# Kernel optimization log

Hardware: AMD Instinct MI355X
Metric: run time of the kernel (lower is better)

The kernel has to match this reference:

```python
import jax, jax.numpy as jnp
import numpy as np
from math import pi as PI

L = 8192      # sequence length
D = 512       # feature dim
EMAS = 8      # number of decay rates


def setup_inputs() -> dict:
    key = jax.random.key(0)
    k1, _ = jax.random.split(key)
    x = jax.random.normal(k1, (L, D), dtype=jnp.float32)
    # module initializes log_decay = linspace(-pi, pi, emas)
    log_decay = jnp.linspace(-PI, PI, EMAS, dtype=jnp.float32)
    return {"x": x, "log_decay": log_decay}


def reference(x, log_decay):
    decay = jax.nn.sigmoid(log_decay)               # (emas,)
    # initial state: first element broadcast over emas -> (D, emas)
    state = jnp.broadcast_to(x[0][..., None], x.shape[1:] + (EMAS,))

    def ema_step(ema_0, x_1):
        ema_1 = decay * x_1 + (1.0 - decay) * ema_0
        return ema_1, ema_1

    # scan over l; carries (D, emas), xs is x[..., None] -> (L, D, 1) broadcast against decay
    _, ema_x = jax.lax.scan(ema_step, state, x[..., None])
    return ema_x  # (L, D, emas)
```

## Files before the change

### kernel.cpp

```cpp
#include <hip/hip_runtime.h>
#include <math.h>

#define L_   8192
#define D_   512
#define E_   8
#define DE_  4096
#define C_   256
#define LC_  32
#define TD_  128
#define NF4_ (LC_ * TD_ / 4)
#define P2B_ 64

typedef float f4_t __attribute__((ext_vector_type(4)));

__device__ __forceinline__ float sigmoidf_(float v) {
    return 1.0f / (1.0f + expf(-v));
}

__global__ __launch_bounds__(256) void ema_pass1(const float* __restrict__ x,
                                                 const float* __restrict__ ld,
                                                 float* __restrict__ contrib) {
    __shared__ f4_t tile[NF4_];
    const int c = blockIdx.x >> 2;
    const int q = blockIdx.x & 3;
    const int t = threadIdx.x;

    const f4_t* xg = (const f4_t*)(x + (size_t)c * LC_ * D_ + q * TD_);
#pragma unroll
    for (int k = 0; k < 4; ++k) {
        const int i = t + 256 * k;
        tile[i] = xg[(size_t)(i >> 5) * (D_ / 4) + (i & 31)];
    }

    const int g  = (q << 8) + t;
    const int dl = t >> 1;
    const int eb = (g & 1) << 2;
    float a[4], b[4];
#pragma unroll
    for (int e = 0; e < 4; ++e) { a[e] = sigmoidf_(ld[eb + e]); b[e] = 1.0f - a[e]; }

    __syncthreads();

    const float* tl = (const float*)tile;
    float s[4] = {0.f, 0.f, 0.f, 0.f};
#pragma unroll
    for (int r = 0; r < LC_; ++r) {
        const float xv = tl[r * TD_ + dl];
#pragma unroll
        for (int e = 0; e < 4; ++e) s[e] = fmaf(b[e], s[e], a[e] * xv);
    }
    f4_t rr = {s[0], s[1], s[2], s[3]};
    *(f4_t*)(contrib + (size_t)c * DE_ + 4 * g) = rr;
}

__global__ __launch_bounds__(P2B_) void ema_pass2(const float* __restrict__ x,
                                                  const float* __restrict__ ld,
                                                  const float* __restrict__ contrib,
                                                  float* __restrict__ states) {
    const int chain = blockIdx.x * P2B_ + threadIdx.x;
    const int d = chain >> 3;
    const int e = chain & 7;
    const float a = sigmoidf_(ld[e]);
    float B = 1.0f - a;
#pragma unroll
    for (int k = 0; k < 5; ++k) B *= B;

    float cb[2][32];
#pragma unroll
    for (int j = 0; j < 32; ++j) cb[0][j] = contrib[(size_t)j * DE_ + chain];

    float s = x[d];
    states[chain] = s;

#pragma unroll
    for (int gr = 0; gr < C_ / 32; ++gr) {
        if (gr + 1 < C_ / 32) {
#pragma unroll
            for (int j = 0; j < 32; ++j)
                cb[(gr + 1) & 1][j] = contrib[(size_t)((gr + 1) * 32 + j) * DE_ + chain];
        }
#pragma unroll
        for (int j = 0; j < 32; ++j) {
            s = fmaf(B, s, cb[gr & 1][j]);
            states[(size_t)(gr * 32 + j + 1) * DE_ + chain] = s;
        }
    }
}

__global__ __launch_bounds__(256) void ema_pass3(const float* __restrict__ x,
                                                 const float* __restrict__ ld,
                                                 const float* __restrict__ states,
                                                 float* __restrict__ out) {
    __shared__ f4_t tile[NF4_];
    const int c = blockIdx.x >> 2;
    const int q = blockIdx.x & 3;
    const int t = threadIdx.x;

    const f4_t* xg = (const f4_t*)(x + (size_t)c * LC_ * D_ + q * TD_);
#pragma unroll
    for (int k = 0; k < 4; ++k) {
        const int i = t + 256 * k;
        tile[i] = xg[(size_t)(i >> 5) * (D_ / 4) + (i & 31)];
    }

    const int g  = (q << 8) + t;
    const int dl = t >> 1;
    const int eb = (g & 1) << 2;
    float a[4], b[4];
#pragma unroll
    for (int e = 0; e < 4; ++e) { a[e] = sigmoidf_(ld[eb + e]); b[e] = 1.0f - a[e]; }

    f4_t y = *(const f4_t*)(states + (size_t)c * DE_ + 4 * g);
    float* op = out + (size_t)c * LC_ * DE_ + 4 * g;

    __syncthreads();

    const float* tl = (const float*)tile;
#pragma unroll
    for (int r = 0; r < LC_; ++r) {
        const float xv = tl[r * TD_ + dl];
        y.x = fmaf(b[0], y.x, a[0] * xv);
        y.y = fmaf(b[1], y.y, a[1] * xv);
        y.z = fmaf(b[2], y.z, a[2] * xv);
        y.w = fmaf(b[3], y.w, a[3] * xv);
        *(f4_t*)(op + (size_t)r * DE_) = y;
    }
}

__global__ __launch_bounds__(256) void ema_naive(const float* __restrict__ x,
                                                 const float* __restrict__ ld,
                                                 float* __restrict__ out) {
    const int chain = blockIdx.x * 256 + threadIdx.x;
    const int d = chain >> 3;
    const int e = chain & 7;
    const float a = sigmoidf_(ld[e]);
    const float b = 1.0f - a;
    float y = x[d];
    for (int l = 0; l < L_; ++l) {
        y = fmaf(b, y, a * x[(size_t)l * D_ + d]);
        out[(size_t)l * DE_ + chain] = y;
    }
}

extern "C" void kernel_launch(void* const* d_in, const int* in_sizes, int n_in,
                              void* d_out, int out_size, void* d_ws, size_t ws_size,
                              hipStream_t stream) {
    const float* x  = (const float*)d_in[0];
    const float* ld = (const float*)d_in[1];
    float* out = (float*)d_out;

    const size_t need = (size_t)(2 * C_ + 1) * DE_ * sizeof(float);
    if (ws_size >= need) {
        float* contrib = (float*)d_ws;
        float* states  = contrib + (size_t)C_ * DE_;
        ema_pass1<<<C_ * 4, 256, 0, stream>>>(x, ld, contrib);
        ema_pass2<<<DE_ / P2B_, P2B_, 0, stream>>>(x, ld, contrib, states);
        ema_pass3<<<C_ * 4, 256, 0, stream>>>(x, ld, states, out);
    } else {
        ema_naive<<<DE_ / 256, 256, 0, stream>>>(x, ld, out);
    }
}
```

Measured before the change: 158.9 us.

## Fuse three-pass chunked EMA scan into one cooperative kernel with hierarchical prefix

Replaces the three separate launches (chunk contributions, serial cross-chunk scan, chunk expansion) with one cooperative kernel that uses grid-wide syncs between phases. The serial cross-chunk scan becomes two levels: group aggregates over 16 chunks, a short serial scan over 16 groups, then each block rolls forward through up to 15 chunk contributions. The x tile stays in shared memory across phases, so it is not reloaded. This removes launch gaps and shortens the long serial pass2 chain, at the cost of three grid barriers and a cooperative launch of 1024 blocks that must all be resident; if that launch fails, the code falls back to the old three-kernel path.

```diff
diff --git a/kernel.cpp b/kernel.cpp
--- a/kernel.cpp
+++ b/kernel.cpp
@@ -1,5 +1,8 @@
 #include <hip/hip_runtime.h>
+#include <hip/hip_cooperative_groups.h>
 #include <math.h>
+
+namespace cg = cooperative_groups;
 
 #define L_   8192
 #define D_   512
@@ -9,12 +12,128 @@
 #define LC_  32
 #define TD_  128
 #define NF4_ (LC_ * TD_ / 4)
+#define GRP_ 16
+#define NG_  (C_ / GRP_)
 #define P2B_ 64
 
 typedef float f4_t __attribute__((ext_vector_type(4)));
 
 __device__ __forceinline__ float sigmoidf_(float v) {
     return 1.0f / (1.0f + expf(-v));
+}
+
+__global__ __launch_bounds__(256, 4) void ema_fused(const float* __restrict__ x,
+                                                    const float* __restrict__ ld,
+                                                    float* __restrict__ contrib,
+                                                    float* __restrict__ gagg,
+                                                    float* __restrict__ gpref,
+                                                    float* __restrict__ out) {
+    cg::grid_group grid = cg::this_grid();
+    __shared__ f4_t tile[NF4_];
+    const int b = blockIdx.x;
+    const int c = b >> 2;
+    const int q = b & 3;
+    const int t = threadIdx.x;
+
+    const f4_t* xg = (const f4_t*)(x + (size_t)c * LC_ * D_ + q * TD_);
+#pragma unroll
+    for (int k = 0; k < 4; ++k) {
+        const int i = t + 256 * k;
+        tile[i] = xg[(size_t)(i >> 5) * (D_ / 4) + (i & 31)];
+    }
+
+    const int g  = (q << 8) + t;
+    const int dl = t >> 1;
+    const int eb = (g & 1) << 2;
+    float a[4], bb[4];
+#pragma unroll
+    for (int e = 0; e < 4; ++e) { a[e] = sigmoidf_(ld[eb + e]); bb[e] = 1.0f - a[e]; }
+
+    __syncthreads();
+    const float* tl = (const float*)tile;
+    {
+        float s[4] = {0.f, 0.f, 0.f, 0.f};
+#pragma unroll
+        for (int r = 0; r < LC_; ++r) {
+            const float xv = tl[r * TD_ + dl];
+#pragma unroll
+            for (int e = 0; e < 4; ++e) s[e] = fmaf(bb[e], s[e], a[e] * xv);
+        }
+        f4_t rr = {s[0], s[1], s[2], s[3]};
+        *(f4_t*)(contrib + (size_t)c * DE_ + 4 * g) = rr;
+    }
+
+    grid.sync();
+
+    if (b < 256) {
+        const int tid   = b * 256 + t;
+        const int chain = tid & (DE_ - 1);
+        const int grp   = tid >> 12;
+        const float ae  = sigmoidf_(ld[chain & 7]);
+        float B = 1.0f - ae;
+#pragma unroll
+        for (int k = 0; k < 5; ++k) B *= B;
+        float G = 0.f;
+#pragma unroll
+        for (int j = 0; j < GRP_; ++j)
+            G = fmaf(B, G, contrib[(size_t)(grp * GRP_ + j) * DE_ + chain]);
+        gagg[(size_t)grp * DE_ + chain] = G;
+    }
+
+    grid.sync();
+
+    if (b < 16) {
+        const int chain = b * 256 + t;
+        const int d = chain >> 3;
+        const float ae = sigmoidf_(ld[chain & 7]);
+        float B = 1.0f - ae;
+#pragma unroll
+        for (int k = 0; k < 5; ++k) B *= B;
+        float B16 = B;
+#pragma unroll
+        for (int k = 0; k < 4; ++k) B16 *= B16;
+        float S = x[d];
+        for (int grp = 0; grp < NG_; ++grp) {
+            gpref[(size_t)grp * DE_ + chain] = S;
+            S = fmaf(B16, S, gagg[(size_t)grp * DE_ + chain]);
+        }
+    }
+
+    grid.sync();
+
+    {
+        const int grp = c >> 4;
+        const int off = c & (GRP_ - 1);
+        float B[4];
+#pragma unroll
+        for (int e = 0; e < 4; ++e) {
+            float v = bb[e];
+#pragma unroll
+            for (int k = 0; k < 5; ++k) v *= v;
+            B[e] = v;
+        }
+        f4_t S = *(const f4_t*)(gpref + (size_t)grp * DE_ + 4 * g);
+        float y0 = S.x, y1 = S.y, y2 = S.z, y3 = S.w;
+        for (int cc = grp * GRP_; cc < grp * GRP_ + off; ++cc) {
+            f4_t gc = *(const f4_t*)(contrib + (size_t)cc * DE_ + 4 * g);
+            y0 = fmaf(B[0], y0, gc.x);
+            y1 = fmaf(B[1], y1, gc.y);
+            y2 = fmaf(B[2], y2, gc.z);
+            y3 = fmaf(B[3], y3, gc.w);
+        }
+
+        float* op = out + (size_t)c * LC_ * DE_ + 4 * g;
+#pragma unroll
+        for (int r = 0; r < LC_; ++r) {
+            const float xv = tl[r * TD_ + dl];
+            y0 = fmaf(bb[0], y0, a[0] * xv);
+            y1 = fmaf(bb[1], y1, a[1] * xv);
+            y2 = fmaf(bb[2], y2, a[2] * xv);
+            y3 = fmaf(bb[3], y3, a[3] * xv);
+            f4_t yy = {y0, y1, y2, y3};
+            *(f4_t*)(op + (size_t)r * DE_) = yy;
+        }
+    }
 }
 
 __global__ __launch_bounds__(256) void ema_pass1(const float* __restrict__ x,
@@ -31,16 +150,13 @@
         const int i = t + 256 * k;
         tile[i] = xg[(size_t)(i >> 5) * (D_ / 4) + (i & 31)];
     }
-
     const int g  = (q << 8) + t;
     const int dl = t >> 1;
     const int eb = (g & 1) << 2;
     float a[4], b[4];
 #pragma unroll
     for (int e = 0; e < 4; ++e) { a[e] = sigmoidf_(ld[eb + e]); b[e] = 1.0f - a[e]; }
-
     __syncthreads();
-
     const float* tl = (const float*)tile;
     float s[4] = {0.f, 0.f, 0.f, 0.f};
 #pragma unroll
@@ -64,14 +180,11 @@
     float B = 1.0f - a;
 #pragma unroll
     for (int k = 0; k < 5; ++k) B *= B;
-
     float cb[2][32];
 #pragma unroll
     for (int j = 0; j < 32; ++j) cb[0][j] = contrib[(size_t)j * DE_ + chain];
-
     float s = x[d];
     states[chain] = s;
-
 #pragma unroll
     for (int gr = 0; gr < C_ / 32; ++gr) {
         if (gr + 1 < C_ / 32) {
@@ -102,19 +215,15 @@
         const int i = t + 256 * k;
         tile[i] = xg[(size_t)(i >> 5) * (D_ / 4) + (i & 31)];
     }
-
     const int g  = (q << 8) + t;
     const int dl = t >> 1;
     const int eb = (g & 1) << 2;
     float a[4], b[4];
 #pragma unroll
     for (int e = 0; e < 4; ++e) { a[e] = sigmoidf_(ld[eb + e]); b[e] = 1.0f - a[e]; }
-
     f4_t y = *(const f4_t*)(states + (size_t)c * DE_ + 4 * g);
     float* op = out + (size_t)c * LC_ * DE_ + 4 * g;
-
     __syncthreads();
-
     const float* tl = (const float*)tile;
 #pragma unroll
     for (int r = 0; r < LC_; ++r) {
@@ -149,13 +258,24 @@
     const float* ld = (const float*)d_in[1];
     float* out = (float*)d_out;
 
-    const size_t need = (size_t)(2 * C_ + 1) * DE_ * sizeof(float);
+    const size_t rows = (size_t)C_ + 2 * NG_ + (C_ + 1);
+    const size_t need = rows * DE_ * sizeof(float);
     if (ws_size >= need) {
         float* contrib = (float*)d_ws;
-        float* states  = contrib + (size_t)C_ * DE_;
-        ema_pass1<<<C_ * 4, 256, 0, stream>>>(x, ld, contrib);
-        ema_pass2<<<DE_ / P2B_, P2B_, 0, stream>>>(x, ld, contrib, states);
-        ema_pass3<<<C_ * 4, 256, 0, stream>>>(x, ld, states, out);
+        float* gagg    = contrib + (size_t)C_ * DE_;
+        float* gpref   = gagg    + (size_t)NG_ * DE_;
+        float* states  = gpref   + (size_t)NG_ * DE_;
+
+        void* args[] = {(void*)&x, (void*)&ld, (void*)&contrib,
+                        (void*)&gagg, (void*)&gpref, (void*)&out};
+        hipError_t err = hipLaunchCooperativeKernel(
+            reinterpret_cast<void*>(ema_fused), dim3(C_ * 4), dim3(256),
+            args, 0, stream);
+        if (err != hipSuccess) {
+            ema_pass1<<<C_ * 4, 256, 0, stream>>>(x, ld, contrib);
+            ema_pass2<<<DE_ / P2B_, P2B_, 0, stream>>>(x, ld, contrib, states);
+            ema_pass3<<<C_ * 4, 256, 0, stream>>>(x, ld, states, out);
+        }
     } else {
         ema_naive<<<DE_ / 256, 256, 0, stream>>>(x, ld, out);
     }
```

Result: slower. 432.1 us (+171.9%).

## Replace serial chunk-state scan with two-level group aggregation

Applied to the files above, without the earlier changes.

The middle pass was a serial scan over 256 chunks run by only 4096 threads. It is replaced by a parallel kernel that folds the chunk contributions of each 16-chunk group into a group aggregate. The output kernel then rebuilds its starting state from the group aggregates (decay^512 steps) and the chunk contributions inside its own group (decay^32 steps). This removes a long, latency-bound sequential kernel, at the cost of extra redundant reads of the aggregates and contributions in the output kernel.

```diff
diff --git a/kernel.cpp b/kernel.cpp
--- a/kernel.cpp
+++ b/kernel.cpp
@@ -9,7 +9,8 @@
 #define LC_  32
 #define TD_  128
 #define NF4_ (LC_ * TD_ / 4)
-#define P2B_ 64
+#define GRP_ 16
+#define NG_  (C_ / GRP_)
 
 typedef float f4_t __attribute__((ext_vector_type(4)));
 
@@ -17,9 +18,9 @@
     return 1.0f / (1.0f + expf(-v));
 }
 
-__global__ __launch_bounds__(256) void ema_pass1(const float* __restrict__ x,
-                                                 const float* __restrict__ ld,
-                                                 float* __restrict__ contrib) {
+__global__ __launch_bounds__(256) void ema_contrib(const float* __restrict__ x,
+                                                   const float* __restrict__ ld,
+                                                   float* __restrict__ contrib) {
     __shared__ f4_t tile[NF4_];
     const int c = blockIdx.x >> 2;
     const int q = blockIdx.x & 3;
@@ -53,44 +54,29 @@
     *(f4_t*)(contrib + (size_t)c * DE_ + 4 * g) = rr;
 }
 
-__global__ __launch_bounds__(P2B_) void ema_pass2(const float* __restrict__ x,
-                                                  const float* __restrict__ ld,
-                                                  const float* __restrict__ contrib,
-                                                  float* __restrict__ states) {
-    const int chain = blockIdx.x * P2B_ + threadIdx.x;
-    const int d = chain >> 3;
-    const int e = chain & 7;
-    const float a = sigmoidf_(ld[e]);
-    float B = 1.0f - a;
+__global__ __launch_bounds__(256) void ema_gagg(const float* __restrict__ ld,
+                                                const float* __restrict__ contrib,
+                                                float* __restrict__ gagg) {
+    const int tid = blockIdx.x * 256 + threadIdx.x;
+    const int ch  = tid & (DE_ - 1);
+    const int grp = tid >> 12;
+    const float a = sigmoidf_(ld[ch & 7]);
+    float B32 = 1.0f - a;
 #pragma unroll
-    for (int k = 0; k < 5; ++k) B *= B;
+    for (int k = 0; k < 5; ++k) B32 *= B32;
 
-    float cb[2][32];
+    float G = 0.f;
 #pragma unroll
-    for (int j = 0; j < 32; ++j) cb[0][j] = contrib[(size_t)j * DE_ + chain];
-
-    float s = x[d];
-    states[chain] = s;
-
-#pragma unroll
-    for (int gr = 0; gr < C_ / 32; ++gr) {
-        if (gr + 1 < C_ / 32) {
-#pragma unroll
-            for (int j = 0; j < 32; ++j)
-                cb[(gr + 1) & 1][j] = contrib[(size_t)((gr + 1) * 32 + j) * DE_ + chain];
-        }
-#pragma unroll
-        for (int j = 0; j < 32; ++j) {
-            s = fmaf(B, s, cb[gr & 1][j]);
-            states[(size_t)(gr * 32 + j + 1) * DE_ + chain] = s;
-        }
-    }
+    for (int j = 0; j < GRP_; ++j)
+        G = fmaf(B32, G, contrib[(size_t)(grp * GRP_ + j) * DE_ + ch]);
+    gagg[(size_t)grp * DE_ + ch] = G;
 }
 
-__global__ __launch_bounds__(256) void ema_pass3(const float* __restrict__ x,
-                                                 const float* __restrict__ ld,
-                                                 const float* __restrict__ states,
-                                                 float* __restrict__ out) {
+__global__ __launch_bounds__(256) void ema_out(const float* __restrict__ x,
+                                               const float* __restrict__ ld,
+                                               const float* __restrict__ contrib,
+                                               const float* __restrict__ gagg,
+                                               float* __restrict__ out) {
     __shared__ f4_t tile[NF4_];
     const int c = blockIdx.x >> 2;
     const int q = blockIdx.x & 3;
@@ -105,25 +91,53 @@
 
     const int g  = (q << 8) + t;
     const int dl = t >> 1;
+    const int d  = g >> 1;
     const int eb = (g & 1) << 2;
-    float a[4], b[4];
+    float a[4], b[4], B32[4], B512[4];
 #pragma unroll
-    for (int e = 0; e < 4; ++e) { a[e] = sigmoidf_(ld[eb + e]); b[e] = 1.0f - a[e]; }
+    for (int e = 0; e < 4; ++e) {
+        a[e] = sigmoidf_(ld[eb + e]);
+        b[e] = 1.0f - a[e];
+        float v = b[e];
+#pragma unroll
+        for (int k = 0; k < 5; ++k) v *= v;
+        B32[e] = v;
+#pragma unroll
+        for (int k = 0; k < 4; ++k) v *= v;
+        B512[e] = v;
+    }
 
-    f4_t y = *(const f4_t*)(states + (size_t)c * DE_ + 4 * g);
+    const int grp = c >> 4;
+    const float x0 = x[d];
+    float y0 = x0, y1 = x0, y2 = x0, y3 = x0;
+    for (int h = 0; h < grp; ++h) {
+        f4_t gv = *(const f4_t*)(gagg + (size_t)h * DE_ + 4 * g);
+        y0 = fmaf(B512[0], y0, gv.x);
+        y1 = fmaf(B512[1], y1, gv.y);
+        y2 = fmaf(B512[2], y2, gv.z);
+        y3 = fmaf(B512[3], y3, gv.w);
+    }
+    for (int cc = grp * GRP_; cc < c; ++cc) {
+        f4_t pv = *(const f4_t*)(contrib + (size_t)cc * DE_ + 4 * g);
+        y0 = fmaf(B32[0], y0, pv.x);
+        y1 = fmaf(B32[1], y1, pv.y);
+        y2 = fmaf(B32[2], y2, pv.z);
+        y3 = fmaf(B32[3], y3, pv.w);
+    }
+
     float* op = out + (size_t)c * LC_ * DE_ + 4 * g;
-
     __syncthreads();
 
     const float* tl = (const float*)tile;
 #pragma unroll
     for (int r = 0; r < LC_; ++r) {
         const float xv = tl[r * TD_ + dl];
-        y.x = fmaf(b[0], y.x, a[0] * xv);
-        y.y = fmaf(b[1], y.y, a[1] * xv);
-        y.z = fmaf(b[2], y.z, a[2] * xv);
-        y.w = fmaf(b[3], y.w, a[3] * xv);
-        *(f4_t*)(op + (size_t)r * DE_) = y;
+        y0 = fmaf(b[0], y0, a[0] * xv);
+        y1 = fmaf(b[1], y1, a[1] * xv);
+        y2 = fmaf(b[2], y2, a[2] * xv);
+        y3 = fmaf(b[3], y3, a[3] * xv);
+        f4_t yy = {y0, y1, y2, y3};
+        *(f4_t*)(op + (size_t)r * DE_) = yy;
     }
 }
 
@@ -149,13 +163,13 @@
     const float* ld = (const float*)d_in[1];
     float* out = (float*)d_out;
 
-    const size_t need = (size_t)(2 * C_ + 1) * DE_ * sizeof(float);
+    const size_t need = (size_t)(C_ + NG_) * DE_ * sizeof(float);
     if (ws_size >= need) {
         float* contrib = (float*)d_ws;
-        float* states  = contrib + (size_t)C_ * DE_;
-        ema_pass1<<<C_ * 4, 256, 0, stream>>>(x, ld, contrib);
-        ema_pass2<<<DE_ / P2B_, P2B_, 0, stream>>>(x, ld, contrib, states);
-        ema_pass3<<<C_ * 4, 256, 0, stream>>>(x, ld, states, out);
+        float* gagg    = contrib + (size_t)C_ * DE_;
+        ema_contrib<<<C_ * 4, 256, 0, stream>>>(x, ld, contrib);
+        ema_gagg<<<NG_ * DE_ / 256, 256, 0, stream>>>(ld, contrib, gagg);
+        ema_out<<<C_ * 4, 256, 0, stream>>>(x, ld, contrib, gagg, out);
     } else {
         ema_naive<<<DE_ / 256, 256, 0, stream>>>(x, ld, out);
     }
```

New measurement: 151.6 us. 1.05x faster.
